# Kernel optimization log

Measured on AMD Instinct MI355X. Metric: run time of the kernel, lower is better.

## Reference

```python
import jax, jax.numpy as jnp
import numpy as np

BLOCK_SIZE = 64
R_BLOCKS = 64          # r: number of rotation blocks (r * block_size == in_features)
N_ELEMENTS = BLOCK_SIZE * (BLOCK_SIZE - 1) // 2  # 2016
NUM_NEUMANN_TERMS = 5

# strict upper-triangular indices (matches torch.triu_indices(b, b, 1))
_ROWS, _COLS = np.triu_indices(BLOCK_SIZE, 1)


def _cayley_neumann(weight):
    """weight: (r, n_elements) -> batch of orthogonal-ish blocks (r, b, b)."""
    b = BLOCK_SIZE
    M = jnp.zeros((weight.shape[0], b, b), dtype=weight.dtype)
    M = M.at[:, _ROWS, _COLS].set(weight)
    Q = M - jnp.swapaxes(M, -1, -2)           # skew-symmetric (r, b, b)
    I = jnp.eye(b, dtype=weight.dtype)
    # R = I + 2Q + 2Q^2 + ... + 2Q^(terms-1)
    R = I + 2.0 * Q
    Qp = jnp.matmul(Q, Q)
    R = R + 2.0 * Qp
    for _ in range(3, NUM_NEUMANN_TERMS):
        Qp = jnp.matmul(Qp, Q)
        R = R + 2.0 * Qp
    return R


def setup_inputs() -> dict:
    key = jax.random.key(0)
    k_x, k_w = jax.random.split(key)
    x = jax.random.normal(k_x, (8192, 4096), dtype=jnp.float32)
    # small weights so the Neumann series approximates the Cayley transform
    weight = jax.random.normal(k_w, (R_BLOCKS, N_ELEMENTS), dtype=jnp.float32) * 0.01
    return {"x": x, "weight": weight}


def reference(x, weight):
    # x: (N, in_features); block-diagonal rotation applied per 64-wide block
    orth = _cayley_neumann(weight)                      # (r, b, b)
    N = x.shape[0]
    xr = x.reshape(N, R_BLOCKS, BLOCK_SIZE)             # (N, r, b)
    out = jnp.einsum("nrk,rkc->nrc", xr, orth)          # block-diag matmul
    return out.reshape(x.shape)
```

## Files before the change

### kernel.cpp

```cpp
#include <hip/hip_runtime.h>


#define BS 64
#define NW 2016
#define LDP 68


__device__ __forceinline__ void mm_tile_68(const float (*A)[LDP], const float (*Bm)[LDP],
                                           int r0, int c0, float p[4][4]) {
  for (int k = 0; k < 64; k += 4) {
    float4 bv[4], av[4];
#pragma unroll
    for (int u = 0; u < 4; ++u) bv[u] = *(const float4*)&Bm[k + u][c0];
#pragma unroll
    for (int i = 0; i < 4; ++i) av[i] = *(const float4*)&A[r0 + i][k];
#pragma unroll
    for (int u = 0; u < 4; ++u) {
      const float4 b = bv[u];
#pragma unroll
      for (int i = 0; i < 4; ++i) {
        const float a = ((const float*)&av[i])[u];
        p[i][0] += a * b.x;
        p[i][1] += a * b.y;
        p[i][2] += a * b.z;
        p[i][3] += a * b.w;
      }
    }
  }
}

__global__ __launch_bounds__(256) void oft_build_R(const float* __restrict__ w,
                                                   float* __restrict__ Rout) {
  const int r = blockIdx.x;
  const int t = threadIdx.x;
  __shared__ float Q[BS][LDP];
  __shared__ float Pa[BS][LDP];
  __shared__ float Pb[BS][LDP];

  for (int f = t; f < BS * LDP; f += 256) (&Q[0][0])[f] = 0.f;
  __syncthreads();

  for (int i = t; i < NW; i += 256) {
    int row = 0, rem = i;
    while (rem >= 63 - row) { rem -= 63 - row; ++row; }
    const int col = row + 1 + rem;
    const float v = w[r * NW + i];
    Q[row][col] = v;
    Q[col][row] = -v;
  }
  __syncthreads();

  const int tr = t >> 4, tc = t & 15;
  const int r0 = tr * 4, c0 = tc * 4;

  float acc[4][4];
#pragma unroll
  for (int i = 0; i < 4; ++i)
#pragma unroll
    for (int j = 0; j < 4; ++j)
      acc[i][j] = ((r0 + i) == (c0 + j) ? 1.f : 0.f) + 2.f * Q[r0 + i][c0 + j];

  float p[4][4] = {};
  mm_tile_68(Q, Q, r0, c0, p);
#pragma unroll
  for (int i = 0; i < 4; ++i)
#pragma unroll
    for (int j = 0; j < 4; ++j) {
      Pa[r0 + i][c0 + j] = p[i][j];
      acc[i][j] += 2.f * p[i][j];
    }
  __syncthreads();

  float p2[4][4] = {};
  mm_tile_68(Pa, Q, r0, c0, p2);
#pragma unroll
  for (int i = 0; i < 4; ++i)
#pragma unroll
    for (int j = 0; j < 4; ++j) {
      Pb[r0 + i][c0 + j] = p2[i][j];
      acc[i][j] += 2.f * p2[i][j];
    }
  __syncthreads();

  float p3[4][4] = {};
  mm_tile_68(Pb, Q, r0, c0, p3);
#pragma unroll
  for (int i = 0; i < 4; ++i)
#pragma unroll
    for (int j = 0; j < 4; ++j)
      acc[i][j] += 2.f * p3[i][j];

#pragma unroll
  for (int i = 0; i < 4; ++i) {
    float4 v = make_float4(acc[i][0], acc[i][1], acc[i][2], acc[i][3]);
    *(float4*)&Rout[(size_t)r * 4096 + (size_t)(r0 + i) * 64 + c0] = v;
  }
}


__global__ __launch_bounds__(256) void oft_apply(const float* __restrict__ x,
                                                 const float* __restrict__ R,
                                                 float* __restrict__ out) {
  const int r = blockIdx.x;
  const int tile = blockIdx.y;
  const int t = threadIdx.x;

  __shared__ float Rs[BS * BS];
  __shared__ float Xs[BS][LDP];

  const int n0 = tile * 64;

  const float4* Rg = (const float4*)(R + (size_t)r * 4096);
  float4* Rs4 = (float4*)Rs;
#pragma unroll
  for (int i = 0; i < 4; ++i) Rs4[t + 256 * i] = Rg[t + 256 * i];

#pragma unroll
  for (int i = 0; i < 4; ++i) {
    const int f = t + 256 * i;
    const int row = f >> 4;
    const int c4 = (f & 15) << 2;
    *(float4*)&Xs[row][c4] =
        *(const float4*)&x[(size_t)(n0 + row) * 4096 + r * 64 + c4];
  }
  __syncthreads();

  const int tr = t >> 4, tc = t & 15;
  const int c0 = tc * 4, rr0 = tr * 4;

  float acc[4][4] = {};
#pragma unroll 4
  for (int k = 0; k < 64; k += 4) {
    float4 bv[4], av[4];
#pragma unroll
    for (int u = 0; u < 4; ++u) bv[u] = *(const float4*)&Rs[(k + u) * 64 + c0];
#pragma unroll
    for (int i = 0; i < 4; ++i) av[i] = *(const float4*)&Xs[rr0 + i][k];
#pragma unroll
    for (int u = 0; u < 4; ++u) {
      const float4 b = bv[u];
#pragma unroll
      for (int i = 0; i < 4; ++i) {
        const float a = ((const float*)&av[i])[u];
        acc[i][0] += a * b.x;
        acc[i][1] += a * b.y;
        acc[i][2] += a * b.z;
        acc[i][3] += a * b.w;
      }
    }
  }

#pragma unroll
  for (int i = 0; i < 4; ++i) {
    float4 v = make_float4(acc[i][0], acc[i][1], acc[i][2], acc[i][3]);
    *(float4*)&out[(size_t)(n0 + rr0 + i) * 4096 + r * 64 + c0] = v;
  }
}

extern "C" void kernel_launch(void* const* d_in, const int* in_sizes, int n_in,
                              void* d_out, int out_size, void* d_ws, size_t ws_size,
                              hipStream_t stream) {
  const float* x = (const float*)d_in[0];
  const float* w = (const float*)d_in[1];
  float* out = (float*)d_out;
  float* Rws = (float*)d_ws;

  oft_build_R<<<64, 256, 0, stream>>>(w, Rws);
  oft_apply<<<dim3(64, 128), 256, 0, stream>>>(x, Rws, out);
}
```

Measured before the change: 249.5 us.

## Use bf16 MFMA for block-diagonal apply and factor Neumann series

The apply kernel now converts x and R to bf16 and uses 16x16x32 bf16 MFMA instructions instead of scalar FP32 FMAs, processing 128 rows per block. The R build kernel factors the series as Q^2(I+Q+Q^2) to save one matmul, and stores R transposed as packed bf16. The aim is to cut ALU time and R traffic so the kernel is bound by memory bandwidth. The trade is bf16 rounding of both operands, which may exceed tolerance. The output stores are also now scalar and strided rather than float4.

```diff
diff --git a/kernel.cpp b/kernel.cpp
--- a/kernel.cpp
+++ b/kernel.cpp
@@ -1,10 +1,16 @@
 #include <hip/hip_runtime.h>
 
 
-#define BS 64
-#define NW 2016
 #define LDP 68
 
+typedef __attribute__((ext_vector_type(8))) short short8;
+typedef __attribute__((ext_vector_type(4))) float f32x4;
+
+static __device__ __forceinline__ unsigned short f2bf(float f) {
+  unsigned u = __float_as_uint(f);
+  u += 0x7FFF + ((u >> 16) & 1);
+  return (unsigned short)(u >> 16);
+}
 
 __device__ __forceinline__ void mm_tile_68(const float (*A)[LDP], const float (*Bm)[LDP],
                                            int r0, int c0, float p[4][4]) {
@@ -29,36 +35,29 @@
   }
 }
 
+
 __global__ __launch_bounds__(256) void oft_build_R(const float* __restrict__ w,
-                                                   float* __restrict__ Rout) {
+                                                   unsigned* __restrict__ RT) {
   const int r = blockIdx.x;
   const int t = threadIdx.x;
-  __shared__ float Q[BS][LDP];
-  __shared__ float Pa[BS][LDP];
-  __shared__ float Pb[BS][LDP];
+  __shared__ float Q[64][LDP];
+  __shared__ float P[64][LDP];
+  __shared__ float T[64][LDP];
 
-  for (int f = t; f < BS * LDP; f += 256) (&Q[0][0])[f] = 0.f;
+  for (int f = t; f < 64 * LDP; f += 256) (&Q[0][0])[f] = 0.f;
   __syncthreads();
 
-  for (int i = t; i < NW; i += 256) {
+  for (int i = t; i < 2016; i += 256) {
     int row = 0, rem = i;
     while (rem >= 63 - row) { rem -= 63 - row; ++row; }
     const int col = row + 1 + rem;
-    const float v = w[r * NW + i];
+    const float v = w[r * 2016 + i];
     Q[row][col] = v;
     Q[col][row] = -v;
   }
   __syncthreads();
 
-  const int tr = t >> 4, tc = t & 15;
-  const int r0 = tr * 4, c0 = tc * 4;
-
-  float acc[4][4];
-#pragma unroll
-  for (int i = 0; i < 4; ++i)
-#pragma unroll
-    for (int j = 0; j < 4; ++j)
-      acc[i][j] = ((r0 + i) == (c0 + j) ? 1.f : 0.f) + 2.f * Q[r0 + i][c0 + j];
+  const int r0 = (t >> 4) * 4, c0 = (t & 15) * 4;
 
   float p[4][4] = {};
   mm_tile_68(Q, Q, r0, c0, p);
@@ -66,94 +65,109 @@
   for (int i = 0; i < 4; ++i)
 #pragma unroll
     for (int j = 0; j < 4; ++j) {
-      Pa[r0 + i][c0 + j] = p[i][j];
-      acc[i][j] += 2.f * p[i][j];
+      P[r0 + i][c0 + j] = p[i][j];
+      T[r0 + i][c0 + j] = p[i][j] + Q[r0 + i][c0 + j] + ((r0 + i) == (c0 + j) ? 1.f : 0.f);
     }
   __syncthreads();
 
   float p2[4][4] = {};
-  mm_tile_68(Pa, Q, r0, c0, p2);
-#pragma unroll
-  for (int i = 0; i < 4; ++i)
-#pragma unroll
-    for (int j = 0; j < 4; ++j) {
-      Pb[r0 + i][c0 + j] = p2[i][j];
-      acc[i][j] += 2.f * p2[i][j];
-    }
-  __syncthreads();
-
-  float p3[4][4] = {};
-  mm_tile_68(Pb, Q, r0, c0, p3);
+  mm_tile_68(P, T, r0, c0, p2);
+  float acc[4][4];
 #pragma unroll
   for (int i = 0; i < 4; ++i)
 #pragma unroll
     for (int j = 0; j < 4; ++j)
-      acc[i][j] += 2.f * p3[i][j];
+      acc[i][j] = ((r0 + i) == (c0 + j) ? 1.f : 0.f)
+                + 2.f * Q[r0 + i][c0 + j] + 2.f * p2[i][j];
+  __syncthreads();
 
 #pragma unroll
-  for (int i = 0; i < 4; ++i) {
-    float4 v = make_float4(acc[i][0], acc[i][1], acc[i][2], acc[i][3]);
-    *(float4*)&Rout[(size_t)r * 4096 + (size_t)(r0 + i) * 64 + c0] = v;
+  for (int i = 0; i < 4; ++i)
+#pragma unroll
+    for (int j = 0; j < 4; ++j)
+      T[c0 + j][r0 + i] = acc[i][j];
+  __syncthreads();
+
+#pragma unroll
+  for (int i2 = 0; i2 < 8; ++i2) {
+    const int f = t + 256 * i2;
+    const int row = f >> 5, col = (f & 31) * 2;
+    unsigned lo = f2bf(T[row][col]);
+    unsigned hi = f2bf(T[row][col + 1]);
+    RT[(size_t)r * 2048 + f] = lo | (hi << 16);
   }
 }
 
 
 __global__ __launch_bounds__(256) void oft_apply(const float* __restrict__ x,
-                                                 const float* __restrict__ R,
+                                                 const unsigned* __restrict__ RT,
                                                  float* __restrict__ out) {
   const int r = blockIdx.x;
-  const int tile = blockIdx.y;
+  const int n0 = blockIdx.y * 128;
   const int t = threadIdx.x;
 
-  __shared__ float Rs[BS * BS];
-  __shared__ float Xs[BS][LDP];
+  __shared__ __align__(16) unsigned short Xs[128][72];
+  __shared__ __align__(16) unsigned short Rs[64][72];
 
-  const int n0 = tile * 64;
-
-  const float4* Rg = (const float4*)(R + (size_t)r * 4096);
-  float4* Rs4 = (float4*)Rs;
-#pragma unroll
-  for (int i = 0; i < 4; ++i) Rs4[t + 256 * i] = Rg[t + 256 * i];
+  {
+    const uint4* Rg = (const uint4*)(RT + (size_t)r * 2048);
+    uint4 v0 = Rg[t];
+    uint4 v1 = Rg[t + 256];
+    *(uint4*)&Rs[t >> 3][(t & 7) * 8] = v0;
+    *(uint4*)&Rs[(t + 256) >> 3][((t + 256) & 7) * 8] = v1;
+  }
 
 #pragma unroll
-  for (int i = 0; i < 4; ++i) {
+  for (int i = 0; i < 8; ++i) {
     const int f = t + 256 * i;
-    const int row = f >> 4;
-    const int c4 = (f & 15) << 2;
-    *(float4*)&Xs[row][c4] =
-        *(const float4*)&x[(size_t)(n0 + row) * 4096 + r * 64 + c4];
+    const int row = f >> 4, c4 = (f & 15) * 4;
+    float4 v = *(const float4*)&x[(size_t)(n0 + row) * 4096 + r * 64 + c4];
+    ushort4 b;
+    b.x = f2bf(v.x); b.y = f2bf(v.y); b.z = f2bf(v.z); b.w = f2bf(v.w);
+    *(ushort4*)&Xs[row][c4] = b;
   }
   __syncthreads();
 
-  const int tr = t >> 4, tc = t & 15;
-  const int c0 = tc * 4, rr0 = tr * 4;
+  const int lane = t & 63, w = t >> 6;
+  const int lo = lane & 15, q = lane >> 4;
 
-  float acc[4][4] = {};
-#pragma unroll 4
-  for (int k = 0; k < 64; k += 4) {
-    float4 bv[4], av[4];
+  short8 bfr[2][4];
 #pragma unroll
-    for (int u = 0; u < 4; ++u) bv[u] = *(const float4*)&Rs[(k + u) * 64 + c0];
+  for (int h = 0; h < 2; ++h)
 #pragma unroll
-    for (int i = 0; i < 4; ++i) av[i] = *(const float4*)&Xs[rr0 + i][k];
+    for (int c = 0; c < 4; ++c)
+      bfr[h][c] = *(const short8*)&Rs[c * 16 + lo][h * 32 + q * 8];
+
+  f32x4 acc[2][4];
 #pragma unroll
-    for (int u = 0; u < 4; ++u) {
-      const float4 b = bv[u];
+  for (int s2 = 0; s2 < 2; ++s2)
 #pragma unroll
-      for (int i = 0; i < 4; ++i) {
-        const float a = ((const float*)&av[i])[u];
-        acc[i][0] += a * b.x;
-        acc[i][1] += a * b.y;
-        acc[i][2] += a * b.z;
-        acc[i][3] += a * b.w;
-      }
+    for (int c = 0; c < 4; ++c)
+#pragma unroll
+      for (int i = 0; i < 4; ++i) acc[s2][c][i] = 0.f;
+
+#pragma unroll
+  for (int s2 = 0; s2 < 2; ++s2) {
+    const int s = w + 4 * s2;
+#pragma unroll
+    for (int h = 0; h < 2; ++h) {
+      short8 a = *(const short8*)&Xs[s * 16 + lo][h * 32 + q * 8];
+#pragma unroll
+      for (int c = 0; c < 4; ++c)
+        acc[s2][c] = __builtin_amdgcn_mfma_f32_16x16x32_bf16(a, bfr[h][c], acc[s2][c], 0, 0, 0);
     }
   }
 
 #pragma unroll
-  for (int i = 0; i < 4; ++i) {
-    float4 v = make_float4(acc[i][0], acc[i][1], acc[i][2], acc[i][3]);
-    *(float4*)&out[(size_t)(n0 + rr0 + i) * 4096 + r * 64 + c0] = v;
+  for (int s2 = 0; s2 < 2; ++s2) {
+    const int s = w + 4 * s2;
+#pragma unroll
+    for (int c = 0; c < 4; ++c)
+#pragma unroll
+      for (int i = 0; i < 4; ++i) {
+        const int row = n0 + s * 16 + q * 4 + i;
+        out[(size_t)row * 4096 + r * 64 + c * 16 + lo] = acc[s2][c][i];
+      }
   }
 }
 
@@ -163,8 +177,8 @@
   const float* x = (const float*)d_in[0];
   const float* w = (const float*)d_in[1];
   float* out = (float*)d_out;
-  float* Rws = (float*)d_ws;
+  unsigned* RTws = (unsigned*)d_ws;
 
-  oft_build_R<<<64, 256, 0, stream>>>(w, Rws);
-  oft_apply<<<dim3(64, 128), 256, 0, stream>>>(x, Rws, out);
+  oft_build_R<<<64, 256, 0, stream>>>(w, RTws);
+  oft_apply<<<dim3(64, 64), 256, 0, stream>>>(x, RTws, out);
 }
```

Result: no change. 250.4 us (+0.4%).
